# Kernel optimization log

Measured on AMD Instinct MI355X. Metric: run time of the kernel, lower is better.

Reference implementation:

```python
import jax, jax.numpy as jnp
import numpy as np

B, T, I, H, NM = 128, 512, 2, 1024, 8
MS = H // NM  # module size = 128


def setup_inputs() -> dict:
    key = jax.random.key(0)
    ks = jax.random.split(key, 6)
    s = 1.0 / np.sqrt(H)
    return {
        "x": jax.random.normal(ks[0], (B, T + 1, I, 1), jnp.float32),
        "W_ih": jax.random.normal(ks[1], (H, I), jnp.float32) * s,
        "W_hh": jax.random.normal(ks[2], (H, H), jnp.float32) * s,
        "fc_w": jax.random.normal(ks[3], (I, H), jnp.float32) * s,
        "fc_b": jax.random.normal(ks[4], (I,), jnp.float32) * s,
        "enc_w": jax.random.normal(ks[5], (H, I), jnp.float32) * s,
    }


def reference(x, W_ih, W_hh, fc_w, fc_b, enc_w):
    # x: [B, T+1, I, 1] -> squeeze trailing dim
    xs = x[..., 0]                       # [B, T+1, I]
    h0 = xs[:, 0] @ enc_w.T              # start_encoder (no bias) -> [B, H]

    # Clockwork block structure: row-module i reads hidden cols >= i*MS.
    mod_idx = jnp.arange(H) // MS
    mask_hh = (mod_idx[None, :] >= mod_idx[:, None]).astype(W_hh.dtype)
    Whh_m = W_hh * mask_hh               # block upper-triangular recurrent weights
    periods = 2 ** jnp.arange(NM)        # module clock periods [1,2,4,...,128]

    def step(h, inp):
        x_t, t = inp                     # x_t: [B, I], t: scalar step index
        cand = jnp.tanh(x_t @ W_ih.T + h @ Whh_m.T)          # [B, H]
        active = jnp.repeat((t % periods) == 0, MS)          # [H] unit-level clock mask
        h_new = jnp.where(active[None, :], cand, h)          # inactive modules keep state
        return h_new, h_new @ fc_w.T + fc_b                  # fc output per step

    _, outs = jax.lax.scan(step, h0, (jnp.swapaxes(xs[:, 1:], 0, 1), jnp.arange(T)))
    return jnp.swapaxes(outs, 0, 1)      # [B, T, I]
```

## Files before the change

### kernel.cpp

```cpp
#include <hip/hip_runtime.h>
#include <hip/hip_fp16.h>
#include <math.h>

#define Bsz 128
#define Tsz 512
#define Hsz 1024
#define MS  128
#define NT  512


__global__ __launch_bounds__(256)
void retile_whh(const float* __restrict__ W, __half* __restrict__ WBr) {
    const int p = blockIdx.x + 1;
    const int t = threadIdx.x;
    int c = 0;
    while ((c+1)*(c+2)/2 <= p) ++c;
    const int r = p - c*(c+1)/2;
    __half* wb = WBr + (size_t)(p-1) * MS * MS;
    for (int o = t; o < MS*MS; o += 256) {
        const int k  = o >> 12;
        const int tt = (o >> 3) & 511;
        const int e  = o & 7;
        const int row = tt >> 2, jq = tt & 3;
        const int col = jq*32 + (((k + jq) & 3) << 3) + e;
        wb[o] = __float2half(W[(size_t)(r*MS+row)*Hsz + c*MS + col]);
    }
}

__device__ __forceinline__ float fast_tanh(float x) {
    const float e = __expf(2.0f * x);
    return 1.0f - 2.0f * __builtin_amdgcn_rcpf(e + 1.0f);
}

template <int CTRL>
__device__ __forceinline__ float dpp_get(float v) {
    union { float f; int i; } u, o;
    u.f = v;
    o.i = __builtin_amdgcn_update_dpp(0, u.i, CTRL, 0xf, 0xf, true);
    return o.f;
}

__device__ __forceinline__ void pk_fma(float2& acc, float2 a, float2 b) {
    asm("v_pk_fma_f32 %0, %1, %2, %0" : "+v"(acc) : "v"(a), "v"(b));
}

union H4 { short4 s4; __half2 h2[2]; };
union F4 { float4 v; float2 h[2]; };

__global__ __launch_bounds__(NT)
void cwrnn_kernel(const float* __restrict__ x,
                  const float* __restrict__ W_ih,
                  const float* __restrict__ fc_w,
                  const float* __restrict__ fc_b,
                  const float* __restrict__ enc_w,
                  const float* __restrict__ Whh,
                  const __half* __restrict__ WBr,
                  float* __restrict__ out)
{
    __shared__ __half  WL[3*MS*MS];
    __shared__ float   Sp2s[36][MS];
    __shared__ float   h_s[Hsz];
    __shared__ float   H0[2][MS];
    __shared__ float2  x_s[Tsz+1];
    __shared__ float2  wih_s[Hsz];
    __shared__ float2  fcw_s[Hsz];
    __shared__ float2  OpM0[2][8];
    __shared__ float2  OpHi[16];
    __shared__ float2  OpHiN[16];
    __shared__ float   out_s[Tsz*2];

    const int tid   = threadIdx.x;
    const int lane  = tid & 63;
    const int wave  = tid >> 6;
    const int b     = blockIdx.x;
    const int row00 = tid >> 2;
    const int jc    = tid & 3;

    const float2* xb = (const float2*)(x + (size_t)b*(Tsz+1)*2);
    float* outb = out + (size_t)b*Tsz*2;

    for (int i = tid; i < Tsz+1; i += NT) x_s[i] = xb[i];
    for (int i = tid; i < Hsz; i += NT) wih_s[i] = ((const float2*)W_ih)[i];
    for (int i = tid; i < Hsz; i += NT) fcw_s[i] = make_float2(fc_w[i], fc_w[Hsz+i]);
    {
        const int PSEL[3] = {2, 4, 5};
        for (int i = tid; i < 3*MS*MS/8; i += NT) {
            const int pi = i >> 11, rem = i & 2047;
            ((int4*)WL)[i] =
                ((const int4*)(WBr + (size_t)(PSEL[pi]-1)*MS*MS))[rem];
        }
    }
    if (tid < 16) { OpHi[tid] = make_float2(0.f,0.f); OpHiN[tid] = make_float2(0.f,0.f); }
    const float fb0 = fc_b[0], fb1 = fc_b[1];

    F4 w00[8];
    #pragma unroll
    for (int u = 0; u < 8; ++u) {
        const int uu = (u + 2*jc) & 7;
        w00[u].v = *(const float4*)(Whh + (size_t)row00*Hsz + jc*32 + uu*4);
    }
    short4 w01[8], w02[8];
    #pragma unroll
    for (int k = 0; k < 4; ++k) {
        *(int4*)(&w01[2*k]) = *(const int4*)(WBr + (size_t)0*MS*MS + k*4096 + tid*8);
        *(int4*)(&w02[2*k]) = *(const int4*)(WBr + (size_t)2*MS*MS + k*4096 + tid*8);
    }

    {
        const float2 x0 = xb[0];
        for (int i = tid; i < Hsz; i += NT) {
            const float2 ew = ((const float2*)enc_w)[i];
            const float v = x0.x*ew.x + x0.y*ew.y;
            h_s[i] = v;
            if (i < MS) H0[0][i] = v;
        }
    }
    __syncthreads();

    float R1=0.f,R2=0.f,R3=0.f,R4=0.f,R5=0.f,R6=0.f,R7=0.f;

    auto load_hq = [&](int c, F4* hq) {
        #pragma unroll
        for (int u = 0; u < 8; ++u) {
            const int uu = (u + 2*jc) & 7;
            hq[u].v = *(const float4*)(h_s + c*MS + jc*32 + uu*4);
        }
    };
    auto pair_acc16 = [&](const short4* w, const F4* hq) -> float {
        float2 a0 = {0.f,0.f}, a1 = {0.f,0.f};
        #pragma unroll
        for (int u = 0; u < 8; ++u) {
            H4 ww; ww.s4 = w[u];
            pk_fma(a0, __half22float2(ww.h2[0]), hq[u].h[0]);
            pk_fma(a1, __half22float2(ww.h2[1]), hq[u].h[1]);
        }
        return (a0.x + a0.y) + (a1.x + a1.y);
    };
    auto wl_read = [&](int pi, short4* w) {
        const __half* base = WL + (size_t)pi*MS*MS + tid*8;
        #pragma unroll
        for (int k = 0; k < 4; ++k)
            *(int4*)(&w[2*k]) = *(const int4*)(base + k*4096);
    };
    auto wg_load = [&](int p, short4* w) {
        const __half* base = WBr + (size_t)(p-1)*MS*MS + tid*8;
        #pragma unroll
        for (int k = 0; k < 4; ++k)
            *(int4*)(&w[2*k]) = *(const int4*)(base + k*4096);
    };

    auto do_cols = [&](int ashad) {
        F4 hq[8];
        short4 wA[8], wB[8];
        if (ashad >= 3) wg_load(6, wA);
        load_hq(1, hq);
        wl_read(0, wB);
        R1 = pair_acc16(w01, hq);
        { float aa = pair_acc16(wB, hq);
          aa += dpp_get<0xB1>(aa); aa += dpp_get<0x4E>(aa);
          if (jc == 0) Sp2s[2][row00] = aa; }
        if (ashad >= 2) {
            load_hq(2, hq);
            R2 = pair_acc16(w02, hq);
            wl_read(1, wB);
            { float aa = pair_acc16(wB, hq);
              aa += dpp_get<0xB1>(aa); aa += dpp_get<0x4E>(aa);
              if (jc == 0) Sp2s[4][row00] = aa; }
            wl_read(2, wB);
            { float aa = pair_acc16(wB, hq);
              aa += dpp_get<0xB1>(aa); aa += dpp_get<0x4E>(aa);
              if (jc == 0) Sp2s[5][row00] = aa; }
        }
        if (ashad >= 3) {
            load_hq(3, hq);
            int cc = 3, rr = 0;
            while (true) {
                int rn = rr + 1, cn = cc;
                if (rn > cn) { cn += 1; rn = 0; }
                const bool hn = (cn <= ashad);
                if (hn) wg_load(cn*(cn+1)/2 + rn, wB);
                float aa = pair_acc16(wA, hq);
                if (rr == 0) {
                    switch (cc) {
                        case 3: R3 = aa; break;
                        case 4: R4 = aa; break;
                        case 5: R5 = aa; break;
                        case 6: R6 = aa; break;
                        default: R7 = aa; break;
                    }
                } else {
                    aa += dpp_get<0xB1>(aa); aa += dpp_get<0x4E>(aa);
                    if (jc == 0) Sp2s[cc*(cc+1)/2 + rr][row00] = aa;
                }
                if (!hn) break;
                if (cn != cc) load_hq(cn, hq);
                cc = cn; rr = rn;
                #pragma unroll
                for (int u = 0; u < 8; ++u) wA[u] = wB[u];
            }
        }
    };

    do_cols(7);
    __syncthreads();

    for (int t = 0; t < Tsz; ++t) {
        const int A  = (t == 0) ? 7 : ((t & 1) ? 0 : min(__ffs(t)-1, 7));
        const int ap = (t & 1) ? ((t == 1) ? 7 : min(__ffs(t-1)-1, 7)) : 0;
        const float2 xt = x_s[t+1];

        if (ap >= 1) do_cols(ap);

        {
            const float* h0r = H0[t & 1];
            float2 a0 = {0.f,0.f}, a1 = {0.f,0.f};
            #pragma unroll
            for (int u = 0; u < 8; ++u) {
                const int uu = (u + 2*jc) & 7;
                F4 hv; hv.v = *(const float4*)(h0r + jc*32 + uu*4);
                pk_fma(a0, w00[u].h[0], hv.h[0]);
                pk_fma(a1, w00[u].h[1], hv.h[1]);
            }
            float a = (a0.x + a0.y) + (a1.x + a1.y);
            a += ((R1+R2)+(R3+R4)) + ((R5+R6)+R7);
            a += dpp_get<0xB1>(a); a += dpp_get<0x4E>(a);
            const float2 wih0 = wih_s[row00];
            const float hv0 = fast_tanh(a + xt.x*wih0.x + xt.y*wih0.y);
            if (jc == 0) H0[(t+1)&1][row00] = hv0;
            const float2 fw0 = fcw_s[row00];
            float o0 = (jc == 0) ? hv0*fw0.x : 0.f;
            float o1 = (jc == 0) ? hv0*fw0.y : 0.f;
            o0 += dpp_get<0x111>(o0); o1 += dpp_get<0x111>(o1);
            o0 += dpp_get<0x112>(o0); o1 += dpp_get<0x112>(o1);
            o0 += dpp_get<0x114>(o0); o1 += dpp_get<0x114>(o1);
            o0 += dpp_get<0x118>(o0); o1 += dpp_get<0x118>(o1);
            o0 += dpp_get<0x142>(o0); o1 += dpp_get<0x142>(o1);
            o0 += dpp_get<0x143>(o0); o1 += dpp_get<0x143>(o1);
            if (lane == 63) OpM0[t&1][wave] = make_float2(o0, o1);
        }

        if (A >= 1) {
            const int nrows = (A+1)*MS;
            {
                const int g = MS + tid;
                if (g < nrows) {
                    const int r = g >> 7, il = g & (MS-1);
                    float sc[8];
                    #pragma unroll
                    for (int c = 1; c < 8; ++c)
                        sc[c] = Sp2s[c*(c+1)/2 + ((c < r) ? c : r)][il];
                    const float2 wih2 = wih_s[g];
                    float pre = xt.x*wih2.x + xt.y*wih2.y;
                    #pragma unroll
                    for (int c = 1; c < 8; ++c) pre += (c >= r) ? sc[c] : 0.f;
                    const float hv = fast_tanh(pre);
                    h_s[g] = hv;
                    const float2 fw = fcw_s[g];
                    float o0 = hv*fw.x, o1 = hv*fw.y;
                    o0 += dpp_get<0x111>(o0); o1 += dpp_get<0x111>(o1);
                    o0 += dpp_get<0x112>(o0); o1 += dpp_get<0x112>(o1);
                    o0 += dpp_get<0x114>(o0); o1 += dpp_get<0x114>(o1);
                    o0 += dpp_get<0x118>(o0); o1 += dpp_get<0x118>(o1);
                    o0 += dpp_get<0x142>(o0); o1 += dpp_get<0x142>(o1);
                    o0 += dpp_get<0x143>(o0); o1 += dpp_get<0x143>(o1);
                    if (lane == 63) OpHiN[2 + wave] = make_float2(o0, o1);
                }
            }
            {
                const int g = 5*MS + tid;
                if (g < nrows) {
                    const int r = g >> 7, il = g & (MS-1);
                    float sc[8];
                    #pragma unroll
                    for (int c = 1; c < 8; ++c)
                        sc[c] = Sp2s[c*(c+1)/2 + ((c < r) ? c : r)][il];
                    const float2 wih2 = wih_s[g];
                    float pre = xt.x*wih2.x + xt.y*wih2.y;
                    #pragma unroll
                    for (int c = 1; c < 8; ++c) pre += (c >= r) ? sc[c] : 0.f;
                    const float hv = fast_tanh(pre);
                    h_s[g] = hv;
                    const float2 fw = fcw_s[g];
                    float o0 = hv*fw.x, o1 = hv*fw.y;
                    o0 += dpp_get<0x111>(o0); o1 += dpp_get<0x111>(o1);
                    o0 += dpp_get<0x112>(o0); o1 += dpp_get<0x112>(o1);
                    o0 += dpp_get<0x114>(o0); o1 += dpp_get<0x114>(o1);
                    o0 += dpp_get<0x118>(o0); o1 += dpp_get<0x118>(o1);
                    o0 += dpp_get<0x142>(o0); o1 += dpp_get<0x142>(o1);
                    o0 += dpp_get<0x143>(o0); o1 += dpp_get<0x143>(o1);
                    if (lane == 63) OpHiN[10 + wave] = make_float2(o0, o1);
                }
            }
        }

        if (t > 0 && tid == 0) {
            const int tp = t - 1;
            if (ap >= 1) {
                for (int k = 2; k <= 2*ap+1; ++k) OpHi[k] = OpHiN[k];
            }
            float o0 = fb0, o1 = fb1;
            #pragma unroll
            for (int w = 0; w < 8; ++w) { o0 += OpM0[tp&1][w].x; o1 += OpM0[tp&1][w].y; }
            #pragma unroll
            for (int k = 2; k < 16; ++k) { o0 += OpHi[k].x; o1 += OpHi[k].y; }
            out_s[2*tp]   = o0;
            out_s[2*tp+1] = o1;
        }

        __syncthreads();
    }

    if (tid == 0) {
        float o0 = fb0, o1 = fb1;
        #pragma unroll
        for (int w = 0; w < 8; ++w) { o0 += OpM0[1][w].x; o1 += OpM0[1][w].y; }
        #pragma unroll
        for (int k = 2; k < 16; ++k) { o0 += OpHi[k].x; o1 += OpHi[k].y; }
        out_s[2*(Tsz-1)]   = o0;
        out_s[2*(Tsz-1)+1] = o1;
    }
    __syncthreads();
    for (int i = tid; i < Tsz*2; i += NT) outb[i] = out_s[i];
}

extern "C" void kernel_launch(void* const* d_in, const int* in_sizes, int n_in,
                              void* d_out, int out_size, void* d_ws, size_t ws_size,
                              hipStream_t stream) {
    const float* x     = (const float*)d_in[0];
    const float* W_ih  = (const float*)d_in[1];
    const float* W_hh  = (const float*)d_in[2];
    const float* fc_w  = (const float*)d_in[3];
    const float* fc_b  = (const float*)d_in[4];
    const float* enc_w = (const float*)d_in[5];
    float* outp = (float*)d_out;
    __half* WBr = (__half*)((char*)d_ws + 65536);

    retile_whh<<<35, 256, 0, stream>>>(W_hh, WBr);
    cwrnn_kernel<<<Bsz, NT, 0, stream>>>(x, W_ih, fc_w, fc_b, enc_w, W_hh, WBr, outp);
}
```

Measured before the change: 911.4 us.

## Add dedicated waves for high-module tanh/output so they overlap the recurrent matvec

```diff
diff --git a/kernel.cpp b/kernel.cpp
--- a/kernel.cpp
+++ b/kernel.cpp
@@ -6,7 +6,7 @@
 #define Tsz 512
 #define Hsz 1024
 #define MS  128
-#define NT  512
+#define NT  768
 
 
 __global__ __launch_bounds__(256)
@@ -94,16 +94,18 @@
     const float fb0 = fc_b[0], fb1 = fc_b[1];
 
     F4 w00[8];
-    #pragma unroll
-    for (int u = 0; u < 8; ++u) {
-        const int uu = (u + 2*jc) & 7;
-        w00[u].v = *(const float4*)(Whh + (size_t)row00*Hsz + jc*32 + uu*4);
-    }
     short4 w01[8], w02[8];
-    #pragma unroll
-    for (int k = 0; k < 4; ++k) {
-        *(int4*)(&w01[2*k]) = *(const int4*)(WBr + (size_t)0*MS*MS + k*4096 + tid*8);
-        *(int4*)(&w02[2*k]) = *(const int4*)(WBr + (size_t)2*MS*MS + k*4096 + tid*8);
+    if (tid < 512) {
+        #pragma unroll
+        for (int u = 0; u < 8; ++u) {
+            const int uu = (u + 2*jc) & 7;
+            w00[u].v = *(const float4*)(Whh + (size_t)row00*Hsz + jc*32 + uu*4);
+        }
+        #pragma unroll
+        for (int k = 0; k < 4; ++k) {
+            *(int4*)(&w01[2*k]) = *(const int4*)(WBr + (size_t)0*MS*MS + k*4096 + tid*8);
+            *(int4*)(&w02[2*k]) = *(const int4*)(WBr + (size_t)2*MS*MS + k*4096 + tid*8);
+        }
     }
 
     {
@@ -201,7 +203,7 @@
         }
     };
 
-    do_cols(7);
+    if (tid < 512) do_cols(7);
     __syncthreads();
 
     for (int t = 0; t < Tsz; ++t) {
@@ -209,9 +211,9 @@
         const int ap = (t & 1) ? ((t == 1) ? 7 : min(__ffs(t-1)-1, 7)) : 0;
         const float2 xt = x_s[t+1];
 
-        if (ap >= 1) do_cols(ap);
-
-        {
+        if (tid < 512) {
+            if (ap >= 1) do_cols(ap);
+
             const float* h0r = H0[t & 1];
             float2 a0 = {0.f,0.f}, a1 = {0.f,0.f};
             #pragma unroll
@@ -237,80 +239,56 @@
             o0 += dpp_get<0x142>(o0); o1 += dpp_get<0x142>(o1);
             o0 += dpp_get<0x143>(o0); o1 += dpp_get<0x143>(o1);
             if (lane == 63) OpM0[t&1][wave] = make_float2(o0, o1);
-        }
-
-        if (A >= 1) {
-            const int nrows = (A+1)*MS;
-            {
-                const int g = MS + tid;
-                if (g < nrows) {
-                    const int r = g >> 7, il = g & (MS-1);
-                    float sc[8];
-                    #pragma unroll
-                    for (int c = 1; c < 8; ++c)
-                        sc[c] = Sp2s[c*(c+1)/2 + ((c < r) ? c : r)][il];
-                    const float2 wih2 = wih_s[g];
-                    float pre = xt.x*wih2.x + xt.y*wih2.y;
-                    #pragma unroll
-                    for (int c = 1; c < 8; ++c) pre += (c >= r) ? sc[c] : 0.f;
-                    const float hv = fast_tanh(pre);
-                    h_s[g] = hv;
-                    const float2 fw = fcw_s[g];
-                    float o0 = hv*fw.x, o1 = hv*fw.y;
-                    o0 += dpp_get<0x111>(o0); o1 += dpp_get<0x111>(o1);
-                    o0 += dpp_get<0x112>(o0); o1 += dpp_get<0x112>(o1);
-                    o0 += dpp_get<0x114>(o0); o1 += dpp_get<0x114>(o1);
-                    o0 += dpp_get<0x118>(o0); o1 += dpp_get<0x118>(o1);
-                    o0 += dpp_get<0x142>(o0); o1 += dpp_get<0x142>(o1);
-                    o0 += dpp_get<0x143>(o0); o1 += dpp_get<0x143>(o1);
-                    if (lane == 63) OpHiN[2 + wave] = make_float2(o0, o1);
+        } else {
+            if (A >= 1) {
+                const int nrows = (A+1)*MS;
+                #pragma unroll
+                for (int p = 0; p < 4; ++p) {
+                    const int g = MS + (tid - 512) + p*256;
+                    if (g < nrows) {
+                        const int r = g >> 7, il = g & (MS-1);
+                        float sc[8];
+                        #pragma unroll
+                        for (int c = 1; c < 8; ++c)
+                            sc[c] = Sp2s[c*(c+1)/2 + ((c < r) ? c : r)][il];
+                        const float2 wih2 = wih_s[g];
+                        float pre = xt.x*wih2.x + xt.y*wih2.y;
+                        #pragma unroll
+                        for (int c = 1; c < 8; ++c) pre += (c >= r) ? sc[c] : 0.f;
+                        const float hv = fast_tanh(pre);
+                        h_s[g] = hv;
+                        const float2 fw = fcw_s[g];
+                        float o0 = hv*fw.x, o1 = hv*fw.y;
+                        o0 += dpp_get<0x111>(o0); o1 += dpp_get<0x111>(o1);
+                        o0 += dpp_get<0x112>(o0); o1 += dpp_get<0x112>(o1);
+                        o0 += dpp_get<0x114>(o0); o1 += dpp_get<0x114>(o1);
+                        o0 += dpp_get<0x118>(o0); o1 += dpp_get<0x118>(o1);
+                        o0 += dpp_get<0x142>(o0); o1 += dpp_get<0x142>(o1);
+                        o0 += dpp_get<0x143>(o0); o1 += dpp_get<0x143>(o1);
+                        if (lane == 63)
+                            OpHiN[2 + (wave - 8) + 4*p] = make_float2(o0, o1);
+                    }
                 }
             }
-            {
-                const int g = 5*MS + tid;
-                if (g < nrows) {
-                    const int r = g >> 7, il = g & (MS-1);
-                    float sc[8];
-                    #pragma unroll
-                    for (int c = 1; c < 8; ++c)
-                        sc[c] = Sp2s[c*(c+1)/2 + ((c < r) ? c : r)][il];
-                    const float2 wih2 = wih_s[g];
-                    float pre = xt.x*wih2.x + xt.y*wih2.y;
-                    #pragma unroll
-                    for (int c = 1; c < 8; ++c) pre += (c >= r) ? sc[c] : 0.f;
-                    const float hv = fast_tanh(pre);
-                    h_s[g] = hv;
-                    const float2 fw = fcw_s[g];
-                    float o0 = hv*fw.x, o1 = hv*fw.y;
-                    o0 += dpp_get<0x111>(o0); o1 += dpp_get<0x111>(o1);
-                    o0 += dpp_get<0x112>(o0); o1 += dpp_get<0x112>(o1);
-                    o0 += dpp_get<0x114>(o0); o1 += dpp_get<0x114>(o1);
-                    o0 += dpp_get<0x118>(o0); o1 += dpp_get<0x118>(o1);
-                    o0 += dpp_get<0x142>(o0); o1 += dpp_get<0x142>(o1);
-                    o0 += dpp_get<0x143>(o0); o1 += dpp_get<0x143>(o1);
-                    if (lane == 63) OpHiN[10 + wave] = make_float2(o0, o1);
+            if (t > 0 && tid == 704) {
+                const int tp = t - 1;
+                if (ap >= 1) {
+                    for (int k = 2; k <= 2*ap+1; ++k) OpHi[k] = OpHiN[k];
                 }
+                float o0 = fb0, o1 = fb1;
+                #pragma unroll
+                for (int w = 0; w < 8; ++w) { o0 += OpM0[tp&1][w].x; o1 += OpM0[tp&1][w].y; }
+                #pragma unroll
+                for (int k = 2; k < 16; ++k) { o0 += OpHi[k].x; o1 += OpHi[k].y; }
+                out_s[2*tp]   = o0;
+                out_s[2*tp+1] = o1;
             }
         }
 
-        if (t > 0 && tid == 0) {
-            const int tp = t - 1;
-            if (ap >= 1) {
-                for (int k = 2; k <= 2*ap+1; ++k) OpHi[k] = OpHiN[k];
-            }
-            float o0 = fb0, o1 = fb1;
-            #pragma unroll
-            for (int w = 0; w < 8; ++w) { o0 += OpM0[tp&1][w].x; o1 += OpM0[tp&1][w].y; }
-            #pragma unroll
-            for (int k = 2; k < 16; ++k) { o0 += OpHi[k].x; o1 += OpHi[k].y; }
-            out_s[2*tp]   = o0;
-            out_s[2*tp+1] = o1;
-        }
-
         __syncthreads();
     }
 
-    if (tid == 0) {
+    if (tid == 704) {
         float o0 = fb0, o1 = fb1;
         #pragma unroll
         for (int w = 0; w < 8; ++w) { o0 += OpM0[1][w].x; o1 += OpM0[1][w].y; }
```

After: 1.578 ms. +73.2%, slower.
